# Performance work log

Hardware: AMD Instinct MI355X
Metric: run time of the kernel (lower is better)

Reference implementation:

```python
import jax, jax.numpy as jnp
import numpy as np
from jax import lax

CHAR_EMB = 30      # char_embedding_dim
N_FILT = 30        # num_cnn_filter (depthwise multiplier)
KSIZE = 3          # char_kernel_size
WORD_EMB = 100     # word_embedding_dim
MAX_WLEN = 40      # max_word_len
N_CHARS = 102      # characters.id + 2
VOCAB = 400002     # GloVe 400k + unk + pad


def setup_inputs() -> dict:
    key = jax.random.key(0)
    k1, k2, k3, k4, k5, k6 = jax.random.split(key, 6)
    B, S = 64, 128
    char_ids = jax.random.randint(k1, (B, S, MAX_WLEN), 0, N_CHARS)
    word_ids = jax.random.randint(k2, (B, S), 0, VOCAB)
    bound = (3.0 / CHAR_EMB) ** 0.5
    char_emb = jax.random.uniform(k3, (N_CHARS, CHAR_EMB), minval=-bound, maxval=bound, dtype=jnp.float32)
    # grouped Conv1d: out=CHAR_EMB*N_FILT=900, in_per_group=1, kernel=3 (OIH layout)
    fan = 1 * KSIZE + N_FILT * KSIZE
    xav = (6.0 / fan) ** 0.5
    conv_w = jax.random.uniform(k4, (CHAR_EMB * N_FILT, 1, KSIZE), minval=-xav, maxval=xav, dtype=jnp.float32)
    conv_b = jnp.zeros((CHAR_EMB * N_FILT,), dtype=jnp.float32)
    glove = jax.random.normal(k5, (VOCAB, WORD_EMB), dtype=jnp.float32)
    return {"char_ids": char_ids, "word_ids": word_ids, "char_emb": char_emb,
            "conv_w": conv_w, "conv_b": conv_b, "glove": glove}


def reference(char_ids, word_ids, char_emb, conv_w, conv_b, glove):
    B, S, W = char_ids.shape
    # char embedding lookup: [B,S,W,E] -> NCH layout [B*S, E, W]
    x = char_emb[char_ids]                       # [B,S,W,30]
    x = jnp.transpose(x, (0, 1, 3, 2)).reshape(B * S, CHAR_EMB, W)
    # depthwise (grouped) conv, groups=30, multiplier=30 -> 900 out channels, length W-K+1
    y = lax.conv_general_dilated(
        x, conv_w, window_strides=(1,), padding="VALID",
        dimension_numbers=("NCH", "OIH", "NCH"),
        feature_group_count=CHAR_EMB)            # [B*S, 900, 38]
    y = y + conv_b[None, :, None]
    pooled = jnp.max(y, axis=2).reshape(B, S, CHAR_EMB * N_FILT)  # max-over-time
    glove_e = glove[word_ids]                    # [B,S,100]
    return jnp.concatenate([pooled, glove_e], axis=2)  # [B,S,1000]
```

## Files before the change

kernel.cpp:

```cpp
#include <hip/hip_runtime.h>

#define CHAR_EMB 30
#define NFILT    30
#define WLEN     40
#define TOUT     38
#define OUTC     900
#define WORD_EMB 100
#define RP2      42

typedef float f32x2 __attribute__((ext_vector_type(2)));
typedef float f32x4 __attribute__((ext_vector_type(4)));

__device__ __forceinline__ f32x2 pk_fma(f32x2 a, f32x2 b, f32x2 c) {
    f32x2 d;
    asm("v_pk_fma_f32 %0, %1, %2, %3" : "=v"(d) : "v"(a), "v"(b), "v"(c));
    return d;
}
__device__ __forceinline__ f32x2 pk_mul(f32x2 a, f32x2 b) {
    f32x2 d;
    asm("v_pk_mul_f32 %0, %1, %2" : "=v"(d) : "v"(a), "v"(b));
    return d;
}
__device__ __forceinline__ float max3f(float a, float b, float c) {
    float d;
    asm("v_max3_f32 %0, %1, %2, %3" : "=v"(d) : "v"(a), "v"(b), "v"(c));
    return d;
}

__global__ __launch_bounds__(256, 4) void encoder_kernel(
    const int*   __restrict__ char_ids,
    const int*   __restrict__ word_ids,
    const float* __restrict__ char_emb,
    const float* __restrict__ conv_w,
    const float* __restrict__ conv_b,
    const float* __restrict__ glove,
    float*       __restrict__ out,
    int BS)
{
    const int nA   = 2 * blockIdx.x;
    const int nB   = nA + 1;
    const bool hasB = (nB < BS);
    const int tid  = threadIdx.x;

    __shared__ int cid[2 * WLEN];
    __shared__ __align__(16) f32x2 xs[CHAR_EMB * RP2];

    float* orowA = out + (long)nA * (OUTC + WORD_EMB);
    float* orowB = out + (long)nB * (OUTC + WORD_EMB);

    if (tid < 2 * WLEN) {
        cid[tid] = (tid < WLEN || hasB) ? char_ids[nA * WLEN + tid] : 0;
    }
    __syncthreads();

    for (int i = tid; i < WLEN * CHAR_EMB; i += 256) {
        const int t = i / CHAR_EMB;
        const int c = i - t * CHAR_EMB;
        const float a = char_emb[cid[t] * CHAR_EMB + c];
        const float b = char_emb[cid[WLEN + t] * CHAR_EMB + c];
        f32x2 v; v.x = a; v.y = b;
        xs[c * RP2 + t] = v;
    }
    __syncthreads();

    if (tid < 240) {
        const int g = tid >> 3;
        const int j = tid & 7;

        f32x2 W0[4], W1[4], W2[4];
        float bias[4];
        int   oc[4];
        #pragma unroll
        for (int u = 0; u < 4; ++u) {
            const int f = j + 8 * u;
            float w0 = 0.f, w1 = 0.f, w2 = 0.f, bb = 0.f;
            if (f < NFILT) {
                const int o = g * NFILT + f;
                oc[u] = o;
                w0 = conv_w[o * 3 + 0];
                w1 = conv_w[o * 3 + 1];
                w2 = conv_w[o * 3 + 2];
                bb = conv_b[o];
            } else {
                oc[u] = -1;
            }
            W0[u].x = w0; W0[u].y = w0;
            W1[u].x = w1; W1[u].y = w1;
            W2[u].x = w2; W2[u].y = w2;
            bias[u] = bb;
        }

        f32x2 m[4];
        #pragma unroll
        for (int u = 0; u < 4; ++u) { m[u].x = -3.4e38f; m[u].y = -3.4e38f; }

        const f32x4* rp = reinterpret_cast<const f32x4*>(&xs[g * RP2]);

        {
            f32x4 q[11];
            #pragma unroll
            for (int k = 0; k < 11; ++k) q[k] = rp[k];
            #define XA(t) (((t) & 1) ? q[(t) >> 1].zw : q[(t) >> 1].xy)
            #pragma unroll
            for (int i = 0; i < 10; ++i) {
                const f32x2 x0 = XA(2 * i + 0);
                const f32x2 x1 = XA(2 * i + 1);
                const f32x2 x2 = XA(2 * i + 2);
                const f32x2 x3 = XA(2 * i + 3);
                #pragma unroll
                for (int u = 0; u < 4; ++u) {
                    const f32x2 v0 = pk_fma(W0[u], x0, pk_fma(W1[u], x1, pk_mul(W2[u], x2)));
                    const f32x2 v1 = pk_fma(W0[u], x1, pk_fma(W1[u], x2, pk_mul(W2[u], x3)));
                    m[u].x = max3f(m[u].x, v0.x, v1.x);
                    m[u].y = max3f(m[u].y, v0.y, v1.y);
                }
            }
            #undef XA
        }

        {
            f32x4 q[10];
            #pragma unroll
            for (int k = 0; k < 10; ++k) q[k] = rp[10 + k];
            #define XB(s) (((s) & 1) ? q[(s) >> 1].zw : q[(s) >> 1].xy)
            #pragma unroll
            for (int i = 0; i < 9; ++i) {
                const int s = 2 * i;
                const f32x2 x0 = XB(s + 0);
                const f32x2 x1 = XB(s + 1);
                const f32x2 x2 = XB(s + 2);
                const f32x2 x3 = XB(s + 3);
                #pragma unroll
                for (int u = 0; u < 4; ++u) {
                    const f32x2 v0 = pk_fma(W0[u], x0, pk_fma(W1[u], x1, pk_mul(W2[u], x2)));
                    const f32x2 v1 = pk_fma(W0[u], x1, pk_fma(W1[u], x2, pk_mul(W2[u], x3)));
                    m[u].x = max3f(m[u].x, v0.x, v1.x);
                    m[u].y = max3f(m[u].y, v0.y, v1.y);
                }
            }
            #undef XB
        }

        #pragma unroll
        for (int u = 0; u < 4; ++u) {
            if (oc[u] >= 0) {
                orowA[oc[u]] = m[u].x + bias[u];
                if (hasB) orowB[oc[u]] = m[u].y + bias[u];
            }
        }
    } else {
        const int k = tid - 240;
        {
            const f32x4* gp = reinterpret_cast<const f32x4*>(glove + (long)word_ids[nA] * WORD_EMB);
            f32x4* op = reinterpret_cast<f32x4*>(orowA + OUTC);
            #pragma unroll
            for (int q = 0; q < 2; ++q) {
                const int idx = k + 16 * q;
                if (idx < WORD_EMB / 4) op[idx] = gp[idx];
            }
        }
        if (hasB) {
            const f32x4* gp = reinterpret_cast<const f32x4*>(glove + (long)word_ids[nB] * WORD_EMB);
            f32x4* op = reinterpret_cast<f32x4*>(orowB + OUTC);
            #pragma unroll
            for (int q = 0; q < 2; ++q) {
                const int idx = k + 16 * q;
                if (idx < WORD_EMB / 4) op[idx] = gp[idx];
            }
        }
    }
}

extern "C" void kernel_launch(void* const* d_in, const int* in_sizes, int n_in,
                              void* d_out, int out_size, void* d_ws, size_t ws_size,
                              hipStream_t stream) {
    const int*   char_ids = (const int*)  d_in[0];
    const int*   word_ids = (const int*)  d_in[1];
    const float* char_emb = (const float*)d_in[2];
    const float* conv_w   = (const float*)d_in[3];
    const float* conv_b   = (const float*)d_in[4];
    const float* glove    = (const float*)d_in[5];
    float*       out      = (float*)      d_out;

    const int BS = in_sizes[1];
    const int nblk = (BS + 1) / 2;

    encoder_kernel<<<nblk, 256, 0, stream>>>(
        char_ids, word_ids, char_emb, conv_w, conv_b, glove, out, BS);
}
```

Measured before the change: 228.5 us.

## Raise occupancy target, vectorize char-embedding gather, stream conv inputs through registers

The launch bound's minimum blocks per SM rises from 4 to 8. The main conv loop is restructured to slide a two-register window over LDS rows instead of preloading 11 vec4 values into registers, which cuts register pressure so the higher occupancy fits. The char embedding gather now loads pairs of floats per thread, halving the number of gather iterations, and output-channel indices are recomputed at store time instead of being kept in registers. The risk is more LDS reads per iteration inside a partially unrolled loop, which could cost latency if the added occupancy does not hide it.

```diff
diff --git a/kernel.cpp b/kernel.cpp
--- a/kernel.cpp
+++ b/kernel.cpp
@@ -27,7 +27,7 @@
     return d;
 }
 
-__global__ __launch_bounds__(256, 4) void encoder_kernel(
+__global__ __launch_bounds__(256, 8) void encoder_kernel(
     const int*   __restrict__ char_ids,
     const int*   __restrict__ word_ids,
     const float* __restrict__ char_emb,
@@ -53,13 +53,16 @@
     }
     __syncthreads();
 
-    for (int i = tid; i < WLEN * CHAR_EMB; i += 256) {
-        const int t = i / CHAR_EMB;
-        const int c = i - t * CHAR_EMB;
-        const float a = char_emb[cid[t] * CHAR_EMB + c];
-        const float b = char_emb[cid[WLEN + t] * CHAR_EMB + c];
-        f32x2 v; v.x = a; v.y = b;
-        xs[c * RP2 + t] = v;
+    for (int i = tid; i < WLEN * (CHAR_EMB / 2); i += 256) {
+        const int t  = i / (CHAR_EMB / 2);
+        const int cp = i - t * (CHAR_EMB / 2);
+        const int c  = 2 * cp;
+        const f32x2 a = *reinterpret_cast<const f32x2*>(char_emb + cid[t] * CHAR_EMB + c);
+        const f32x2 b = *reinterpret_cast<const f32x2*>(char_emb + cid[WLEN + t] * CHAR_EMB + c);
+        f32x2 v0; v0.x = a.x; v0.y = b.x;
+        f32x2 v1; v1.x = a.y; v1.y = b.y;
+        xs[(c    ) * RP2 + t] = v0;
+        xs[(c + 1) * RP2 + t] = v1;
     }
     __syncthreads();
 
@@ -69,20 +72,16 @@
 
         f32x2 W0[4], W1[4], W2[4];
         float bias[4];
-        int   oc[4];
         #pragma unroll
         for (int u = 0; u < 4; ++u) {
             const int f = j + 8 * u;
             float w0 = 0.f, w1 = 0.f, w2 = 0.f, bb = 0.f;
             if (f < NFILT) {
                 const int o = g * NFILT + f;
-                oc[u] = o;
                 w0 = conv_w[o * 3 + 0];
                 w1 = conv_w[o * 3 + 1];
                 w2 = conv_w[o * 3 + 2];
                 bb = conv_b[o];
-            } else {
-                oc[u] = -1;
             }
             W0[u].x = w0; W0[u].y = w0;
             W1[u].x = w1; W1[u].y = w1;
@@ -95,57 +94,32 @@
         for (int u = 0; u < 4; ++u) { m[u].x = -3.4e38f; m[u].y = -3.4e38f; }
 
         const f32x4* rp = reinterpret_cast<const f32x4*>(&xs[g * RP2]);
-
-        {
-            f32x4 q[11];
+        f32x4 cur = rp[0];
+        #pragma unroll 2
+        for (int k = 0; k < 19; ++k) {
+            const f32x4 nxt = rp[k + 1];
+            const f32x2 x0 = cur.xy;
+            const f32x2 x1 = cur.zw;
+            const f32x2 x2 = nxt.xy;
+            const f32x2 x3 = nxt.zw;
             #pragma unroll
-            for (int k = 0; k < 11; ++k) q[k] = rp[k];
-            #define XA(t) (((t) & 1) ? q[(t) >> 1].zw : q[(t) >> 1].xy)
-            #pragma unroll
-            for (int i = 0; i < 10; ++i) {
-                const f32x2 x0 = XA(2 * i + 0);
-                const f32x2 x1 = XA(2 * i + 1);
-                const f32x2 x2 = XA(2 * i + 2);
-                const f32x2 x3 = XA(2 * i + 3);
-                #pragma unroll
-                for (int u = 0; u < 4; ++u) {
-                    const f32x2 v0 = pk_fma(W0[u], x0, pk_fma(W1[u], x1, pk_mul(W2[u], x2)));
-                    const f32x2 v1 = pk_fma(W0[u], x1, pk_fma(W1[u], x2, pk_mul(W2[u], x3)));
-                    m[u].x = max3f(m[u].x, v0.x, v1.x);
-                    m[u].y = max3f(m[u].y, v0.y, v1.y);
-                }
+            for (int u = 0; u < 4; ++u) {
+                const f32x2 v0 = pk_fma(W0[u], x0, pk_fma(W1[u], x1, pk_mul(W2[u], x2)));
+                const f32x2 v1 = pk_fma(W0[u], x1, pk_fma(W1[u], x2, pk_mul(W2[u], x3)));
+                m[u].x = max3f(m[u].x, v0.x, v1.x);
+                m[u].y = max3f(m[u].y, v0.y, v1.y);
             }
-            #undef XA
-        }
-
-        {
-            f32x4 q[10];
-            #pragma unroll
-            for (int k = 0; k < 10; ++k) q[k] = rp[10 + k];
-            #define XB(s) (((s) & 1) ? q[(s) >> 1].zw : q[(s) >> 1].xy)
-            #pragma unroll
-            for (int i = 0; i < 9; ++i) {
-                const int s = 2 * i;
-                const f32x2 x0 = XB(s + 0);
-                const f32x2 x1 = XB(s + 1);
-                const f32x2 x2 = XB(s + 2);
-                const f32x2 x3 = XB(s + 3);
-                #pragma unroll
-                for (int u = 0; u < 4; ++u) {
-                    const f32x2 v0 = pk_fma(W0[u], x0, pk_fma(W1[u], x1, pk_mul(W2[u], x2)));
-                    const f32x2 v1 = pk_fma(W0[u], x1, pk_fma(W1[u], x2, pk_mul(W2[u], x3)));
-                    m[u].x = max3f(m[u].x, v0.x, v1.x);
-                    m[u].y = max3f(m[u].y, v0.y, v1.y);
-                }
-            }
-            #undef XB
+            cur = nxt;
         }
 
         #pragma unroll
         for (int u = 0; u < 4; ++u) {
-            if (oc[u] >= 0) {
-                orowA[oc[u]] = m[u].x + bias[u];
-                if (hasB) orowB[oc[u]] = m[u].y + bias[u];
+            const int f = j + 8 * u;
+            if (f < NFILT) {
+                const int o = g * NFILT + f;
+                const float bb = bias[u];
+                orowA[o] = m[u].x + bb;
+                if (hasB) orowB[o] = m[u].y + bb;
             }
         }
     } else {
```

Result: no change. 228.3 us (-0.1%).
